# Kernel tuning notes

Measured on AMD Instinct MI355X. Metric: run time of the kernel, lower is better.

The kernel has to match this reference:

```python
import jax, jax.numpy as jnp
import numpy as np

EMBED_DIM = 1024
NUM_HEADS = 16
HEAD_DIM = EMBED_DIM // NUM_HEADS


def setup_inputs() -> dict:
    key = jax.random.key(0)
    k1, k2, k3, k4, k5 = jax.random.split(key, 5)
    B, S, D = 2, 2048, EMBED_DIM
    s_in = 1.0 / np.sqrt(D)
    x = jax.random.normal(k1, (B, S, D), dtype=jnp.float32)
    W_qkv = jax.random.uniform(k2, (D, 3 * D), dtype=jnp.float32, minval=-s_in, maxval=s_in)
    b_qkv = jax.random.uniform(k3, (3 * D,), dtype=jnp.float32, minval=-s_in, maxval=s_in)
    W_out = jax.random.uniform(k4, (D, D), dtype=jnp.float32, minval=-s_in, maxval=s_in)
    b_out = jax.random.uniform(k5, (D,), dtype=jnp.float32, minval=-s_in, maxval=s_in)
    return {"x": x, "W_qkv": W_qkv, "b_qkv": b_qkv, "W_out": W_out, "b_out": b_out}


def reference(x, W_qkv, b_qkv, W_out, b_out):
    B, S, D = x.shape
    H, Hd = NUM_HEADS, HEAD_DIM
    qkv = x @ W_qkv + b_qkv                      # [B,S,3D]
    qkv = qkv.reshape(B, S, 3, H, Hd)
    q = qkv[:, :, 0].transpose(0, 2, 1, 3)       # [B,H,S,Hd]
    k = qkv[:, :, 1].transpose(0, 2, 1, 3)
    v = qkv[:, :, 2].transpose(0, 2, 1, 3)
    scores = jnp.einsum('bhsd,bhtd->bhst', q, k) / jnp.sqrt(jnp.float32(Hd))
    attn = jax.nn.softmax(scores, axis=-1)       # dropout is identity in eval mode
    out = jnp.einsum('bhst,bhtd->bhsd', attn, v)
    out = out.transpose(0, 2, 1, 3).reshape(B, S, D)
    return out @ W_out + b_out
```

## Files before the change

### kernel.cpp

```cpp
#include <hip/hip_runtime.h>
#include <stdint.h>
#include <math.h>

#define EMBED 1024
#define HEADS 16
#define HDIM  64
#define SEQ   2048
#define BATCH 2

typedef __bf16 bf16x8 __attribute__((ext_vector_type(8)));
typedef float  f32x4  __attribute__((ext_vector_type(4)));
typedef unsigned short u16x8 __attribute__((ext_vector_type(8)));
typedef unsigned short u16x4 __attribute__((ext_vector_type(4)));
typedef uint32_t u32x4v __attribute__((ext_vector_type(4)));

static __device__ __forceinline__ unsigned short f2bf(float f){
  union { float f; uint32_t u; } v; v.f = f;
  uint32_t u = v.u;
  uint32_t r = (u + 0x7FFFu + ((u >> 16) & 1u)) >> 16;
  return (unsigned short)r;
}
static __device__ __forceinline__ bf16x8 as_bf(u16x8 v){ return __builtin_bit_cast(bf16x8, v); }

static __device__ __forceinline__ uint32_t pk_bf16(float a, float b){
#if defined(__has_builtin) && __has_builtin(__builtin_amdgcn_cvt_pk_bf16_f32)
  typedef __bf16 bf16x2 __attribute__((ext_vector_type(2)));
  bf16x2 p = __builtin_amdgcn_cvt_pk_bf16_f32(a, b);
  return __builtin_bit_cast(uint32_t, p);
#else
  return (uint32_t)f2bf(a) | ((uint32_t)f2bf(b) << 16);
#endif
}

static __device__ __forceinline__ float fexp2(float x){
#if defined(__has_builtin) && __has_builtin(__builtin_amdgcn_exp2f)
  return __builtin_amdgcn_exp2f(x);
#else
  return exp2f(x);
#endif
}

static __device__ __forceinline__ void stage16(const unsigned short* gp,
                                               unsigned short* lp_wave, int lane){
#if defined(__has_builtin) && __has_builtin(__builtin_amdgcn_global_load_lds)
  __builtin_amdgcn_global_load_lds((const __attribute__((address_space(1))) void*)gp,
                                   (__attribute__((address_space(3))) void*)lp_wave,
                                   16, 0, 0);
#else
  *(u16x8*)(lp_wave + lane * 8) = *(const u16x8*)gp;
#endif
}

__global__ __launch_bounds__(256) void prep(
    const float* __restrict__ x,      unsigned short* __restrict__ xb,
    const float* __restrict__ W_qkv,  unsigned short* __restrict__ wqkvT,
    const float* __restrict__ W_out,  unsigned short* __restrict__ woutT)
{
  __shared__ unsigned short T[32 * 36];
  const int bid = blockIdx.x;
  const int t   = threadIdx.x;

  if (bid < 4096){
    int i = (bid * 256 + t) * 4;
    float4 v = *(const float4*)(x + i);
    u16x4 o;
    o[0] = f2bf(v.x); o[1] = f2bf(v.y); o[2] = f2bf(v.z); o[3] = f2bf(v.w);
    *(u16x4*)(xb + i) = o;
    return;
  }
  const float* W; unsigned short* Wt; int N, n0, k0;
  if (bid < 7168){
    int idx = bid - 4096;
    W = W_qkv; Wt = wqkvT; N = 3072;
    n0 = (idx % 96) * 32; k0 = (idx / 96) * 32;
  } else {
    int idx = bid - 7168;
    W = W_out; Wt = woutT; N = 1024;
    n0 = (idx & 31) * 32; k0 = (idx >> 5) * 32;
  }
  int kr = t >> 3, nc = (t & 7) * 4;
  float4 wv = *(const float4*)(W + (size_t)(k0 + kr) * N + n0 + nc);
  T[(nc + 0) * 36 + kr] = f2bf(wv.x);
  T[(nc + 1) * 36 + kr] = f2bf(wv.y);
  T[(nc + 2) * 36 + kr] = f2bf(wv.z);
  T[(nc + 3) * 36 + kr] = f2bf(wv.w);
  __syncthreads();
  int nr = t >> 3, kc = (t & 7) * 4;
  *(u16x4*)(Wt + (size_t)(n0 + nr) * 1024 + k0 + kc) = *(const u16x4*)&T[nr * 36 + kc];
}

static __device__ __forceinline__ void gemm_qkv_body(
    int bm, int bn, unsigned short* SM,
    const unsigned short* __restrict__ A,
    const unsigned short* __restrict__ Bt,
    const float* __restrict__ bias,
    unsigned short* __restrict__ q_ws,
    unsigned short* __restrict__ k_ws,
    unsigned short* __restrict__ vt_ws)
{
  unsigned short* As = SM;
  unsigned short* Bs = SM + 8192;
  const int K = 1024;
  const int tid  = threadIdx.x;
  const int w    = tid >> 6, lane = tid & 63;
  const int quad = lane >> 4, l16 = lane & 15;
  const int wm   = (w >> 1) * 64, wn = (w & 1) * 64;

  f32x4 acc[4][4] = {};

  for (int k0 = 0; k0 < K; k0 += 64) {
    #pragma unroll
    for (int i = 0; i < 4; i++){
      int c = w * 4 + i;
      int row = c * 8 + (lane >> 3);
      int kg = (lane & 7) ^ (row & 7);
      stage16(A  + (size_t)(bm * 128 + row) * K + k0 + kg * 8, As + c * 512, lane);
      stage16(Bt + (size_t)(bn * 128 + row) * K + k0 + kg * 8, Bs + c * 512, lane);
    }
    __syncthreads();

    #pragma unroll
    for (int kk = 0; kk < 2; kk++){
      bf16x8 af[4], bfr[4];
      #pragma unroll
      for (int t = 0; t < 4; t++){
        int ra = wm + t * 16 + l16;
        int rb = wn + t * 16 + l16;
        af[t]  = as_bf(*(const u16x8*)&As[(ra << 6) + ((((kk << 2) + quad) ^ (ra & 7)) << 3)]);
        bfr[t] = as_bf(*(const u16x8*)&Bs[(rb << 6) + ((((kk << 2) + quad) ^ (rb & 7)) << 3)]);
      }
      #pragma unroll
      for (int mt = 0; mt < 4; mt++)
        #pragma unroll
        for (int nt = 0; nt < 4; nt++)
          acc[mt][nt] = __builtin_amdgcn_mfma_f32_16x16x32_bf16(af[mt], bfr[nt], acc[mt][nt], 0, 0, 0);
    }
    __syncthreads();
  }

  const int which = (bn * 128) >> 10;
  const int b = bm >> 4;
  const int S_base = (bm & 15) * 128 + wm;

  if (which == 2){
    #pragma unroll
    for (int nt = 0; nt < 4; nt++){
      int gnb = bn * 128 + wn + nt * 16;
      int h   = (gnb & 1023) >> 6;
      int d   = (gnb & 63) + l16;
      float bv = bias[gnb + l16];
      unsigned short* vp = vt_ws + (size_t)(b * HEADS + h) * SEQ * HDIM + (size_t)d * SEQ;
      #pragma unroll
      for (int mt = 0; mt < 4; mt++){
        int spos = S_base + (mt >> 1) * 32 + quad * 8 + (mt & 1) * 4;
        u16x4 o4;
        #pragma unroll
        for (int r = 0; r < 4; r++) o4[r] = f2bf(acc[mt][nt][r] + bv);
        *(u16x4*)(vp + spos) = o4;
      }
    }
    return;
  }

  unsigned short* dst = (which == 0) ? q_ws : k_ws;
  const float scale = (which == 0) ? 0.18033688f : 1.0f;
  #pragma unroll
  for (int nt = 0; nt < 4; nt++){
    int gnb = bn * 128 + wn + nt * 16;
    int h   = (gnb & 1023) >> 6;
    int hd  = (gnb & 63) + l16;
    float bv = bias[gnb + l16];
    unsigned short* dp = dst + (size_t)(b * HEADS + h) * SEQ * HDIM + hd;
    #pragma unroll
    for (int mt = 0; mt < 4; mt++){
      int s0 = S_base + mt * 16 + quad * 4;
      #pragma unroll
      for (int r = 0; r < 4; r++)
        dp[(size_t)(s0 + r) * HDIM] = f2bf((acc[mt][nt][r] + bv) * scale);
    }
  }
}

static __device__ __forceinline__ void gemm_out_body(
    int bm, int bn, unsigned short* SM,
    const unsigned short* __restrict__ A,
    const unsigned short* __restrict__ Bt,
    const float* __restrict__ bias,
    float* __restrict__ Cout)
{
  unsigned short* As = SM;
  unsigned short* Bs = SM + 8192;
  const int K = 1024, N = 1024;
  const int tid  = threadIdx.x;
  const int w    = tid >> 6, lane = tid & 63;
  const int quad = lane >> 4, l16 = lane & 15;
  const int wm   = (w >> 1) * 64, wn = (w & 1) * 32;

  f32x4 acc[4][2] = {};

  for (int k0 = 0; k0 < K; k0 += 64) {
    #pragma unroll
    for (int i = 0; i < 4; i++){
      int c = w * 4 + i;
      int row = c * 8 + (lane >> 3);
      int kg = (lane & 7) ^ (row & 7);
      stage16(A + (size_t)(bm * 128 + row) * K + k0 + kg * 8, As + c * 512, lane);
    }
    #pragma unroll
    for (int i = 0; i < 2; i++){
      int c = w * 2 + i;
      int row = c * 8 + (lane >> 3);
      int kg = (lane & 7) ^ (row & 7);
      stage16(Bt + (size_t)(bn * 64 + row) * K + k0 + kg * 8, Bs + c * 512, lane);
    }
    __syncthreads();

    #pragma unroll
    for (int kk = 0; kk < 2; kk++){
      bf16x8 af[4], bfr[2];
      #pragma unroll
      for (int t = 0; t < 4; t++){
        int ra = wm + t * 16 + l16;
        af[t] = as_bf(*(const u16x8*)&As[(ra << 6) + ((((kk << 2) + quad) ^ (ra & 7)) << 3)]);
      }
      #pragma unroll
      for (int t = 0; t < 2; t++){
        int rb = wn + t * 16 + l16;
        bfr[t] = as_bf(*(const u16x8*)&Bs[(rb << 6) + ((((kk << 2) + quad) ^ (rb & 7)) << 3)]);
      }
      #pragma unroll
      for (int mt = 0; mt < 4; mt++)
        #pragma unroll
        for (int nt = 0; nt < 2; nt++)
          acc[mt][nt] = __builtin_amdgcn_mfma_f32_16x16x32_bf16(af[mt], bfr[nt], acc[mt][nt], 0, 0, 0);
    }
    __syncthreads();
  }

  #pragma unroll
  for (int mt = 0; mt < 4; mt++)
    #pragma unroll
    for (int nt = 0; nt < 2; nt++)
      #pragma unroll
      for (int r = 0; r < 4; r++){
        int gm = bm * 128 + wm + mt * 16 + quad * 4 + r;
        int gn = bn * 64 + wn + nt * 16 + l16;
        Cout[(size_t)gm * N + gn] = acc[mt][nt][r] + bias[gn];
      }
}

static __device__ __forceinline__ void attn_body(
    int abid, int bh_base, unsigned short* SM,
    const unsigned short* __restrict__ q_ws,
    const unsigned short* __restrict__ k_ws,
    const unsigned short* __restrict__ vt_ws,
    unsigned short* __restrict__ o_ws)
{
  unsigned short* Ks  = SM;
  unsigned short* VTs = SM + 8192;
  const int tid  = threadIdx.x;
  const int bh   = bh_base + (abid >> 4);
  const int qt   = abid & 15;
  const int w    = tid >> 6, lane = tid & 63;
  const int quad = lane >> 4, l16 = lane & 15;
  const size_t base = (size_t)bh * SEQ * HDIM;

  bf16x8 bq[2][2];
  #pragma unroll
  for (int mq = 0; mq < 2; mq++){
    int qrow = qt * 128 + w * 32 + mq * 16 + l16;
    #pragma unroll
    for (int ks = 0; ks < 2; ks++)
      bq[mq][ks] = as_bf(*(const u16x8*)(q_ws + base + (size_t)qrow * HDIM + (ks * 4 + quad) * 8));
  }

  const int row0 = w * 16 + (lane >> 3), row1 = row0 + 8;
  const int kg0 = (lane & 7) ^ (row0 & 7), kg1 = (lane & 7) ^ (row1 & 7);
  const int dofs0 = (w * 2) * 512 + lane * 8, dofs1 = dofs0 + 512;

  stage16(k_ws  + base + (size_t)row0 * HDIM + kg0 * 8, Ks  + (w * 2) * 512,     lane);
  stage16(k_ws  + base + (size_t)row1 * HDIM + kg1 * 8, Ks  + (w * 2 + 1) * 512, lane);
  stage16(vt_ws + base + (size_t)row0 * SEQ + kg0 * 8,  VTs + (w * 2) * 512,     lane);
  stage16(vt_ws + base + (size_t)row1 * SEQ + kg1 * 8,  VTs + (w * 2 + 1) * 512, lane);
  __syncthreads();

  const unsigned short* kp0 = k_ws  + base + (size_t)(64 + row0) * HDIM + kg0 * 8;
  const unsigned short* kp1 = k_ws  + base + (size_t)(64 + row1) * HDIM + kg1 * 8;
  const unsigned short* vp0 = vt_ws + base + (size_t)row0 * SEQ + 64 + kg0 * 8;
  const unsigned short* vp1 = vt_ws + base + (size_t)row1 * SEQ + 64 + kg1 * 8;

  f32x4 acc[2][4] = {};
  float li[2] = {0.f, 0.f};

  for (int kt = 0; kt < SEQ / 64; kt++){
    const int co = (kt & 1) * 4096;
    u16x8 kpre0, kpre1, vpre0, vpre1;
    if (kt < SEQ / 64 - 1){
      kpre0 = *(const u16x8*)kp0;  kp0 += 64 * HDIM;
      kpre1 = *(const u16x8*)kp1;  kp1 += 64 * HDIM;
      vpre0 = *(const u16x8*)vp0;  vp0 += 64;
      vpre1 = *(const u16x8*)vp1;  vp1 += 64;
    }

    f32x4 sf[4][2] = {};
    #pragma unroll
    for (int ks = 0; ks < 2; ks++)
      #pragma unroll
      for (int nt = 0; nt < 4; nt++){
        int rk = nt * 16 + l16;
        bf16x8 ak = as_bf(*(const u16x8*)&Ks[co + (rk << 6) + ((((ks << 2) + quad) ^ (rk & 7)) << 3)]);
        #pragma unroll
        for (int mq = 0; mq < 2; mq++)
          sf[nt][mq] = __builtin_amdgcn_mfma_f32_16x16x32_bf16(ak, bq[mq][ks], sf[nt][mq], 0, 0, 0);
      }

    #pragma unroll
    for (int nt = 0; nt < 4; nt++)
      #pragma unroll
      for (int mq = 0; mq < 2; mq++)
        #pragma unroll
        for (int r = 0; r < 4; r++)
          sf[nt][mq][r] = fexp2(sf[nt][mq][r]);
    #pragma unroll
    for (int mq = 0; mq < 2; mq++)
      #pragma unroll
      for (int nt = 0; nt < 4; nt++)
        li[mq] += (sf[nt][mq][0] + sf[nt][mq][1]) + (sf[nt][mq][2] + sf[nt][mq][3]);

    #pragma unroll
    for (int c = 0; c < 2; c++){
      bf16x8 ap[2];
      #pragma unroll
      for (int mq = 0; mq < 2; mq++){
        u32x4v aw;
        aw[0] = pk_bf16(sf[c * 2][mq][0],     sf[c * 2][mq][1]);
        aw[1] = pk_bf16(sf[c * 2][mq][2],     sf[c * 2][mq][3]);
        aw[2] = pk_bf16(sf[c * 2 + 1][mq][0], sf[c * 2 + 1][mq][1]);
        aw[3] = pk_bf16(sf[c * 2 + 1][mq][2], sf[c * 2 + 1][mq][3]);
        ap[mq] = __builtin_bit_cast(bf16x8, aw);
      }
      #pragma unroll
      for (int nt = 0; nt < 4; nt++){
        int rv = nt * 16 + l16;
        bf16x8 bv = as_bf(*(const u16x8*)&VTs[co + (rv << 6) + ((((c << 2) + quad) ^ (rv & 7)) << 3)]);
        #pragma unroll
        for (int mq = 0; mq < 2; mq++)
          acc[mq][nt] = __builtin_amdgcn_mfma_f32_16x16x32_bf16(ap[mq], bv, acc[mq][nt], 0, 0, 0);
      }
    }

    if (kt < SEQ / 64 - 1){
      const int no = (co ^ 4096);
      *(u16x8*)&Ks[no + dofs0]  = kpre0;
      *(u16x8*)&Ks[no + dofs1]  = kpre1;
      *(u16x8*)&VTs[no + dofs0] = vpre0;
      *(u16x8*)&VTs[no + dofs1] = vpre1;
    }
    __syncthreads();
  }

  #pragma unroll
  for (int mq = 0; mq < 2; mq++){
    li[mq] += __shfl_xor(li[mq], 16);
    li[mq] += __shfl_xor(li[mq], 32);
  }
  float inv[2] = {1.0f / li[0], 1.0f / li[1]};
  float invr[2][4];
  #pragma unroll
  for (int mq = 0; mq < 2; mq++)
    #pragma unroll
    for (int r = 0; r < 4; r++)
      invr[mq][r] = __shfl(inv[mq], quad * 4 + r);

  int b = bh >> 4, h = bh & 15;
  #pragma unroll
  for (int mq = 0; mq < 2; mq++)
    #pragma unroll
    for (int nt = 0; nt < 4; nt++)
      #pragma unroll
      for (int r = 0; r < 4; r++){
        int s = qt * 128 + w * 32 + mq * 16 + quad * 4 + r;
        int d = h * 64 + nt * 16 + l16;
        o_ws[((size_t)(b * SEQ + s)) * EMBED + d] = f2bf(acc[mq][nt][r] * invr[mq][r]);
      }
}

__global__ __launch_bounds__(256) void qkv_part(
    const unsigned short* __restrict__ A, const unsigned short* __restrict__ Bt,
    const float* __restrict__ bias,
    unsigned short* q, unsigned short* k, unsigned short* vt, int bm_base)
{
  __shared__ unsigned short SM[16384];
  gemm_qkv_body(bm_base + (blockIdx.x & 15), blockIdx.x >> 4, SM, A, Bt, bias, q, k, vt);
}

__global__ __launch_bounds__(256) void out_part(
    const unsigned short* __restrict__ A, const unsigned short* __restrict__ Bt,
    const float* __restrict__ bias, float* C, int bm_base)
{
  __shared__ unsigned short SM[16384];
  gemm_out_body(bm_base + (blockIdx.x & 15), blockIdx.x >> 4, SM, A, Bt, bias, C);
}

__global__ __launch_bounds__(256) void combo_attn0_qkv1(
    const unsigned short* __restrict__ xb, const unsigned short* __restrict__ wqkvT,
    const float* __restrict__ b_qkv,
    unsigned short* q, unsigned short* k, unsigned short* vt, unsigned short* o)
{
  __shared__ unsigned short SM[16384];
  if (blockIdx.x < 256)
    attn_body(blockIdx.x, 0, SM, q, k, vt, o);
  else {
    int g = blockIdx.x - 256;
    gemm_qkv_body(16 + (g & 15), g >> 4, SM, xb, wqkvT, b_qkv, q, k, vt);
  }
}

__global__ __launch_bounds__(256) void combo_attn1_out0(
    const unsigned short* __restrict__ q, const unsigned short* __restrict__ k,
    const unsigned short* __restrict__ vt, unsigned short* o,
    const unsigned short* __restrict__ woutT, const float* __restrict__ b_out,
    float* out)
{
  __shared__ unsigned short SM[16384];
  if (blockIdx.x < 256)
    attn_body(blockIdx.x, 16, SM, q, k, vt, o);
  else {
    int g = blockIdx.x - 256;
    gemm_out_body(g & 15, g >> 4, SM, o, woutT, b_out, out);
  }
}

extern "C" void kernel_launch(void* const* d_in, const int* in_sizes, int n_in,
                              void* d_out, int out_size, void* d_ws, size_t ws_size,
                              hipStream_t stream) {
  const float* x     = (const float*)d_in[0];
  const float* W_qkv = (const float*)d_in[1];
  const float* b_qkv = (const float*)d_in[2];
  const float* W_out = (const float*)d_in[3];
  const float* b_out = (const float*)d_in[4];
  float* out = (float*)d_out;

  char* ws = (char*)d_ws;
  unsigned short* xb    = (unsigned short*)(ws);
  unsigned short* o     = (unsigned short*)(ws);
  unsigned short* q     = (unsigned short*)(ws + ((size_t)8  << 20));
  unsigned short* k     = (unsigned short*)(ws + ((size_t)16 << 20));
  unsigned short* vt    = (unsigned short*)(ws + ((size_t)24 << 20));
  unsigned short* wqkvT = (unsigned short*)(ws + ((size_t)32 << 20));
  unsigned short* woutT = (unsigned short*)(ws + ((size_t)38 << 20));

  prep<<<dim3(8192), dim3(256), 0, stream>>>(x, xb, W_qkv, wqkvT, W_out, woutT);

  qkv_part<<<dim3(384), dim3(256), 0, stream>>>(xb, wqkvT, b_qkv, q, k, vt, 0);

  combo_attn0_qkv1<<<dim3(640), dim3(256), 0, stream>>>(xb, wqkvT, b_qkv, q, k, vt, o);

  combo_attn1_out0<<<dim3(512), dim3(256), 0, stream>>>(q, k, vt, o, woutT, b_out, out);

  out_part<<<dim3(256), dim3(256), 0, stream>>>(o, woutT, b_out, out, 16);
}
```

Measured before the change: 210.8 us.

## Fuse QKV, attention and out-projection into one persistent kernel with atomic flags

```diff
diff --git a/kernel.cpp b/kernel.cpp
--- a/kernel.cpp
+++ b/kernel.cpp
@@ -51,6 +51,21 @@
 #endif
 }
 
+__device__ int g_flags[4];
+
+static __device__ __forceinline__ void flag_signal(int idx, int tid){
+  __syncthreads();
+  if (tid == 0){ __threadfence(); atomicAdd(&g_flags[idx], 1); }
+}
+static __device__ __forceinline__ void flag_wait(int idx, int target, int tid){
+  if (tid == 0){
+    while (__hip_atomic_load(&g_flags[idx], __ATOMIC_ACQUIRE, __HIP_MEMORY_SCOPE_AGENT) < target)
+      __builtin_amdgcn_s_sleep(8);
+  }
+  __syncthreads();
+  __threadfence();
+}
+
 __global__ __launch_bounds__(256) void prep(
     const float* __restrict__ x,      unsigned short* __restrict__ xb,
     const float* __restrict__ W_qkv,  unsigned short* __restrict__ wqkvT,
@@ -59,6 +74,8 @@
   __shared__ unsigned short T[32 * 36];
   const int bid = blockIdx.x;
   const int t   = threadIdx.x;
+
+  if (bid == 0 && t < 4) g_flags[t] = 0;
 
   if (bid < 4096){
     int i = (bid * 256 + t) * 4;
@@ -140,43 +157,58 @@
 
   const int which = (bn * 128) >> 10;
   const int b = bm >> 4;
-  const int S_base = (bm & 15) * 128 + wm;
+  const int S0 = (bm & 15) * 128;
 
   if (which == 2){
     #pragma unroll
     for (int nt = 0; nt < 4; nt++){
-      int gnb = bn * 128 + wn + nt * 16;
-      int h   = (gnb & 1023) >> 6;
-      int d   = (gnb & 63) + l16;
-      float bv = bias[gnb + l16];
-      unsigned short* vp = vt_ws + (size_t)(b * HEADS + h) * SEQ * HDIM + (size_t)d * SEQ;
+      int coln = wn + nt * 16 + l16;
+      float bv = bias[bn * 128 + coln];
       #pragma unroll
       for (int mt = 0; mt < 4; mt++){
-        int spos = S_base + (mt >> 1) * 32 + quad * 8 + (mt & 1) * 4;
-        u16x4 o4;
-        #pragma unroll
-        for (int r = 0; r < 4; r++) o4[r] = f2bf(acc[mt][nt][r] + bv);
-        *(u16x4*)(vp + spos) = o4;
-      }
-    }
-    return;
-  }
-
-  unsigned short* dst = (which == 0) ? q_ws : k_ws;
-  const float scale = (which == 0) ? 0.18033688f : 1.0f;
-  #pragma unroll
-  for (int nt = 0; nt < 4; nt++){
-    int gnb = bn * 128 + wn + nt * 16;
-    int h   = (gnb & 1023) >> 6;
-    int hd  = (gnb & 63) + l16;
-    float bv = bias[gnb + l16];
-    unsigned short* dp = dst + (size_t)(b * HEADS + h) * SEQ * HDIM + hd;
-    #pragma unroll
-    for (int mt = 0; mt < 4; mt++){
-      int s0 = S_base + mt * 16 + quad * 4;
-      #pragma unroll
-      for (int r = 0; r < 4; r++)
-        dp[(size_t)(s0 + r) * HDIM] = f2bf((acc[mt][nt][r] + bv) * scale);
+        int sposl = wm + (mt >> 1) * 32 + quad * 8 + (mt & 1) * 4;
+        #pragma unroll
+        for (int r = 0; r < 4; r++)
+          SM[coln * 136 + sposl + r] = f2bf(acc[mt][nt][r] + bv);
+      }
+    }
+  } else {
+    const float scale = (which == 0) ? 0.18033688f : 1.0f;
+    #pragma unroll
+    for (int nt = 0; nt < 4; nt++){
+      int coln = wn + nt * 16 + l16;
+      float bv = bias[bn * 128 + coln];
+      #pragma unroll
+      for (int mt = 0; mt < 4; mt++){
+        int sl = wm + mt * 16 + quad * 4;
+        #pragma unroll
+        for (int r = 0; r < 4; r++)
+          SM[(sl + r) * 136 + coln] = f2bf((acc[mt][nt][r] + bv) * scale);
+      }
+    }
+  }
+  __syncthreads();
+
+  if (which == 2){
+    #pragma unroll
+    for (int p = 0; p < 8; p++){
+      int nl = p * 16 + (tid >> 4);
+      int s0 = (tid & 15) * 8;
+      u16x8 v = *(const u16x8*)&SM[nl * 136 + s0];
+      int ng = bn * 128 + nl;
+      int h = (ng & 1023) >> 6, d = ng & 63;
+      *(u16x8*)(vt_ws + (size_t)(b * HEADS + h) * SEQ * HDIM + (size_t)d * SEQ + S0 + s0) = v;
+    }
+  } else {
+    unsigned short* dst = (which == 0) ? q_ws : k_ws;
+    #pragma unroll
+    for (int p = 0; p < 8; p++){
+      int sl = p * 16 + (tid >> 4);
+      int c0 = (tid & 15) * 8;
+      u16x8 v = *(const u16x8*)&SM[sl * 136 + c0];
+      int ng = bn * 128 + c0;
+      int h = (ng & 1023) >> 6, d = ng & 63;
+      *(u16x8*)(dst + (size_t)(b * HEADS + h) * SEQ * HDIM + (size_t)(S0 + sl) * HDIM + d) = v;
     }
   }
 }
@@ -385,49 +417,43 @@
       }
 }
 
-__global__ __launch_bounds__(256) void qkv_part(
-    const unsigned short* __restrict__ A, const unsigned short* __restrict__ Bt,
-    const float* __restrict__ bias,
-    unsigned short* q, unsigned short* k, unsigned short* vt, int bm_base)
-{
-  __shared__ unsigned short SM[16384];
-  gemm_qkv_body(bm_base + (blockIdx.x & 15), blockIdx.x >> 4, SM, A, Bt, bias, q, k, vt);
-}
-
-__global__ __launch_bounds__(256) void out_part(
-    const unsigned short* __restrict__ A, const unsigned short* __restrict__ Bt,
-    const float* __restrict__ bias, float* C, int bm_base)
-{
-  __shared__ unsigned short SM[16384];
-  gemm_out_body(bm_base + (blockIdx.x & 15), blockIdx.x >> 4, SM, A, Bt, bias, C);
-}
-
-__global__ __launch_bounds__(256) void combo_attn0_qkv1(
+__global__ __launch_bounds__(256, 2) void mega(
     const unsigned short* __restrict__ xb, const unsigned short* __restrict__ wqkvT,
     const float* __restrict__ b_qkv,
-    unsigned short* q, unsigned short* k, unsigned short* vt, unsigned short* o)
+    unsigned short* __restrict__ q, unsigned short* __restrict__ k,
+    unsigned short* __restrict__ vt, unsigned short* __restrict__ o,
+    const unsigned short* __restrict__ woutT, const float* __restrict__ b_out,
+    float* __restrict__ out)
 {
-  __shared__ unsigned short SM[16384];
-  if (blockIdx.x < 256)
-    attn_body(blockIdx.x, 0, SM, q, k, vt, o);
-  else {
-    int g = blockIdx.x - 256;
-    gemm_qkv_body(16 + (g & 15), g >> 4, SM, xb, wqkvT, b_qkv, q, k, vt);
-  }
-}
-
-__global__ __launch_bounds__(256) void combo_attn1_out0(
-    const unsigned short* __restrict__ q, const unsigned short* __restrict__ k,
-    const unsigned short* __restrict__ vt, unsigned short* o,
-    const unsigned short* __restrict__ woutT, const float* __restrict__ b_out,
-    float* out)
-{
-  __shared__ unsigned short SM[16384];
-  if (blockIdx.x < 256)
-    attn_body(blockIdx.x, 16, SM, q, k, vt, o);
-  else {
-    int g = blockIdx.x - 256;
-    gemm_out_body(g & 15, g >> 4, SM, o, woutT, b_out, out);
+  __shared__ unsigned short SM[17408];
+  const int bid  = blockIdx.x;
+  const int tid  = threadIdx.x;
+  const int half = bid >> 8;
+
+  {
+    int t1 = bid;
+    gemm_qkv_body(t1 / 24, t1 % 24, SM, xb, wqkvT, b_qkv, q, k, vt);
+    flag_signal(t1 < 384 ? 0 : 1, tid);
+    if (half == 1){
+      __syncthreads();
+      int t2 = bid + 256;
+      gemm_qkv_body(t2 / 24, t2 % 24, SM, xb, wqkvT, b_qkv, q, k, vt);
+      flag_signal(1, tid);
+    }
+  }
+
+  {
+    flag_wait(half, 384, tid);
+    int u = bid & 255;
+    int unit = (u & 7) * 32 + (u >> 3);
+    attn_body(unit, half * 16, SM, q, k, vt, o);
+    flag_signal(2 + half, tid);
+  }
+
+  {
+    flag_wait(2 + half, 256, tid);
+    int u = bid & 255;
+    gemm_out_body(half * 16 + (u >> 4), u & 15, SM, o, woutT, b_out, out);
   }
 }
 
@@ -452,11 +478,6 @@
 
   prep<<<dim3(8192), dim3(256), 0, stream>>>(x, xb, W_qkv, wqkvT, W_out, woutT);
 
-  qkv_part<<<dim3(384), dim3(256), 0, stream>>>(xb, wqkvT, b_qkv, q, k, vt, 0);
-
-  combo_attn0_qkv1<<<dim3(640), dim3(256), 0, stream>>>(xb, wqkvT, b_qkv, q, k, vt, o);
-
-  combo_attn1_out0<<<dim3(512), dim3(256), 0, stream>>>(q, k, vt, o, woutT, b_out, out);
-
-  out_part<<<dim3(256), dim3(256), 0, stream>>>(o, woutT, b_out, out, 16);
-}
+  mega<<<dim3(512), dim3(256), 0, stream>>>(
+      xb, wqkvT, b_qkv, q, k, vt, o, woutT, b_out, out);
+}
```

New measurement: 372.6 us. +76.8%, slower.
